# Performance work log

Hardware: AMD Instinct MI355X
Metric: run time of the kernel (lower is better)

## Reference

```python
import jax, jax.numpy as jnp
import numpy as np

OBS, HID, H, A = 128, 256, 512, 16
T, B = 256, 256


def setup_inputs() -> dict:
    key = jax.random.key(0)
    ks = jax.random.split(key, 8)
    s = lambda k, shape, fan_in: jax.random.normal(k, shape, jnp.float32) / np.sqrt(fan_in).astype(np.float32)
    return {
        "x": jax.random.normal(ks[0], (T, B, OBS), jnp.float32),
        "W_enc": s(ks[1], (OBS, HID), OBS),
        "b_enc": jnp.zeros((HID,), jnp.float32),
        "Wi": s(ks[2], (HID, 4 * H), HID),      # input->gates kernel (i,f,g,o)
        "Wh": s(ks[3], (H, 4 * H), H),          # hidden->gates kernel
        "b_lstm": jnp.zeros((4 * H,), jnp.float32),
        "W_mu": s(ks[4], (H, A), H),
        "b_mu": jnp.zeros((A,), jnp.float32),
        "log_std": jnp.zeros((1, A), jnp.float32),
        "W_v": s(ks[5], (H, 1), H),
        "b_v": jnp.zeros((1,), jnp.float32),
    }


def reference(x, W_enc, b_enc, Wi, Wh, b_lstm, W_mu, b_mu, log_std, W_v, b_v):
    # Encoder MLP: Linear + gelu, mapping obs_dim -> hidden_features.
    feats = jax.nn.gelu(x @ W_enc + b_enc)            # (T, B, HID)
    # Precompute the input contribution to all 4 gates for every timestep
    # (same math as flax OptimizedLSTMCell, hoisted out of the scan).
    x_gates = feats @ Wi + b_lstm                      # (T, B, 4H)
    bsz = x.shape[1]
    c0 = jnp.zeros((bsz, H), x.dtype)
    h0 = jnp.zeros((bsz, H), x.dtype)

    def step(carry, xg):
        c, h = carry
        z = xg + h @ Wh                                # (B, 4H)
        i, f, g, o = jnp.split(z, 4, axis=-1)          # flax gate order i,f,g,o
        c_new = jax.nn.sigmoid(f) * c + jax.nn.sigmoid(i) * jnp.tanh(g)
        h_new = jax.nn.sigmoid(o) * jnp.tanh(c_new)
        return (c_new, h_new), h_new

    _, hs = jax.lax.scan(step, (c0, h0), x_gates)      # hs: (T, B, H)
    # Heads (dropout is identity in eval/deterministic mode).
    mu = hs @ W_mu + b_mu                              # (T, B, A)
    sigma = jnp.broadcast_to(jnp.exp(log_std), mu.shape)
    value = hs @ W_v + b_v                             # (T, B, 1)
    return mu, sigma, value
```

## Files before the change

kernel.cpp:

```cpp
#include <hip/hip_runtime.h>
#include <stdint.h>

#define T_STEPS 256
#define BATCH   256
#define OBS     128
#define HID     256
#define HSZ     512
#define NG      16
#define RPG     16
#define NSLICES 16
#define HCS     32
#define RING_SLOT_W 65536

typedef __attribute__((ext_vector_type(8))) short short8;
typedef __attribute__((ext_vector_type(4))) float f32x4;
typedef __attribute__((ext_vector_type(4))) int   i32x4;

__device__ __forceinline__ unsigned short f2bf(float x) {
    union { float f; uint32_t u; } v; v.f = x;
    uint32_t r = v.u + 0x7FFF + ((v.u >> 16) & 1);
    return (unsigned short)(r >> 16);
}
__device__ __forceinline__ float sigmoidf_(float x) { return 1.f / (1.f + __expf(-x)); }
__device__ __forceinline__ float tanhf_(float x)    { return 1.f - 2.f / (1.f + __expf(2.f * x)); }

__global__ __launch_bounds__(256) void enc_kernel(
    const float* __restrict__ x, const float* __restrict__ W_enc,
    const float* __restrict__ b_enc, unsigned short* __restrict__ feats) {
    __shared__ unsigned short wlds[HID * OBS];
    int tid = threadIdx.x;
    for (int idx = tid; idx < OBS * HID; idx += 256) {
        int k = idx >> 8, n = idx & 255;
        int byte = ((n * OBS + k) * 2) ^ ((n & 7) << 4);
        *(unsigned short*)((char*)wlds + byte) = f2bf(W_enc[k * HID + n]);
    }
    __syncthreads();
    int wave = tid >> 6, lane = tid & 63;
    long m0 = (long)blockIdx.x * 64 + wave * 16;
    int arow = lane & 15, kq = lane >> 4;
    f32x4 acc[16];
    f32x4 z4 = {0.f, 0.f, 0.f, 0.f};
#pragma unroll
    for (int i = 0; i < 16; i++) acc[i] = z4;
#pragma unroll
    for (int kk = 0; kk < OBS; kk += 32) {
        const float* ap = x + (m0 + arow) * OBS + kk + kq * 8;
        float4 a0 = *(const float4*)ap;
        float4 a1 = *(const float4*)(ap + 4);
        short8 af;
        af[0] = (short)f2bf(a0.x); af[1] = (short)f2bf(a0.y);
        af[2] = (short)f2bf(a0.z); af[3] = (short)f2bf(a0.w);
        af[4] = (short)f2bf(a1.x); af[5] = (short)f2bf(a1.y);
        af[6] = (short)f2bf(a1.z); af[7] = (short)f2bf(a1.w);
#pragma unroll
        for (int nt = 0; nt < 16; nt++) {
            int n = nt * 16 + arow;
            int byte = ((n * OBS + kk + kq * 8) * 2) ^ ((n & 7) << 4);
            short8 bf = *(const short8*)((char*)wlds + byte);
            acc[nt] = __builtin_amdgcn_mfma_f32_16x16x32_bf16(af, bf, acc[nt], 0, 0, 0);
        }
    }
#pragma unroll
    for (int nt = 0; nt < 16; nt++) {
        int col = nt * 16 + (lane & 15);
        float bias = b_enc[col];
#pragma unroll
        for (int j = 0; j < 4; j++) {
            long row = m0 + kq * 4 + j;
            float z = acc[nt][j] + bias;
            float zc = 0.79788456f * (z + 0.044715f * z * z * z);
            float g = 0.5f * z * (1.f + tanhf_(zc));
            feats[row * HID + col] = f2bf(g);
        }
    }
}

__global__ __launch_bounds__(256) void prep_wi(
    const float* __restrict__ Wi, unsigned short* __restrict__ Wipk) {
    int t = blockIdx.x * 256 + threadIdx.x;
    int f = t & 15, l = (t >> 4) & 63, w = (t >> 10) & 3, s = t >> 12;
    int ct = f >> 3, i = f & 7;
    int n = w * 32 + ct * 16 + (l & 15);
    int colg = (n & 3) * HSZ + s * HCS + (n >> 2);
    int kbase = i * 32 + (l >> 4) * 8;
    short8 v;
#pragma unroll
    for (int j = 0; j < 8; j++) v[j] = (short)f2bf(Wi[(kbase + j) * 2048 + colg]);
    *(short8*)(Wipk + (long)t * 8) = v;
}

__global__ __launch_bounds__(256) void prep_whimg(
    const float* __restrict__ Wh, unsigned short* __restrict__ WhImg) {
    int t = blockIdx.x * 256 + threadIdx.x;
    int s = t >> 15, r = t & 32767;
    int n = r >> 8, k2 = (r & 255) * 2;
    int colg = (n & 3) * HSZ + s * HCS + (n >> 2);
    unsigned short a = f2bf(Wh[k2 * 2048 + colg]);
    unsigned short b = f2bf(Wh[(k2 + 1) * 2048 + colg]);
    uint32_t w = (uint32_t)a | ((uint32_t)b << 16);
    int P = (n * 1024 + k2 * 2) ^ ((n & 7) << 4);
    *(uint32_t*)((char*)WhImg + s * 131072 + P) = w;
}

__global__ __launch_bounds__(256, 1) void scan_kernel(
    const float* __restrict__ b_lstm, const unsigned short* __restrict__ feats,
    const unsigned short* __restrict__ Wipk, const unsigned short* __restrict__ WhImg,
    uint32_t* __restrict__ ring, uint32_t* __restrict__ flags,
    uint32_t* __restrict__ hs32) {
    __shared__ unsigned short whs[128 * HSZ];
    __shared__ unsigned short hst[RPG * HSZ];
    const int tid = threadIdx.x;
    const int g = blockIdx.x & 15;
    const int slice = blockIdx.x >> 4;
    const int rowg = g * RPG;
    const int wave = tid >> 6, lane = tid & 63;
    const int arow = lane & 15, kq = lane >> 4;

    {
        const i32x4* src = (const i32x4*)((const char*)WhImg + slice * 131072);
        i32x4* dst = (i32x4*)whs;
        for (int idx = tid; idx < 8192; idx += 256) dst[idx] = src[idx];
    }
    short8 wif0[8], wif1[8];
    {
        const short8* wp = (const short8*)Wipk + ((slice * 4 + wave) * 64 + lane) * 16;
#pragma unroll
        for (int i = 0; i < 8; i++) { wif0[i] = wp[i]; wif1[i] = wp[8 + i]; }
    }
    const int a_ = arow >> 2;
    const int hcol0 = slice * HCS + wave * 8 + a_;
    float bl0[4], bl1[4];
#pragma unroll
    for (int q = 0; q < 4; q++) {
        bl0[q] = b_lstm[q * HSZ + hcol0];
        bl1[q] = b_lstm[q * HSZ + hcol0 + 4];
    }
    const int row = kq * 4 + (arow & 3);
    const int colw = slice * 16 + wave * 4 + ((a_ & 1) ? 2 + (a_ >> 1) : (a_ >> 1));
    float c0 = 0.f, c1 = 0.f;
    int wb[4];
#pragma unroll
    for (int j = 0; j < 4; j++) {
        int rj = j * 4 + wave;
        wb[j] = (rj * 1024 + lane * 16) ^ ((rj & 7) << 4);
    }
    short8 ff[8];
    {
        const char* fb = (const char*)feats + ((long)(rowg + arow)) * (HID * 2) + kq * 16;
#pragma unroll
        for (int i = 0; i < 8; i++) ff[i] = *(const short8*)(fb + i * 64);
    }
    f32x4 z4 = {0.f, 0.f, 0.f, 0.f};
    __syncthreads();

    for (int t = 0; t < T_STEPS; ++t) {
        f32x4 acc0 = z4, acc1 = z4;
#pragma unroll
        for (int i = 0; i < 8; i++) {
            acc0 = __builtin_amdgcn_mfma_f32_16x16x32_bf16(ff[i], wif0[i], acc0, 0, 0, 0);
            acc1 = __builtin_amdgcn_mfma_f32_16x16x32_bf16(ff[i], wif1[i], acc1, 0, 0, 0);
        }
        {
            int tn = (t + 1 < T_STEPS) ? t + 1 : t;
            const char* fb = (const char*)feats
                           + ((long)tn * BATCH + rowg + arow) * (HID * 2) + kq * 16;
#pragma unroll
            for (int i = 0; i < 8; i++) ff[i] = *(const short8*)(fb + i * 64);
        }
        __builtin_amdgcn_sched_barrier(0);
        if (t > 0) {
            const uint32_t* fp = flags + ((long)g * T_STEPS + t - 1) * 16 + (lane & 15);
            while (!__all(__hip_atomic_load(fp, __ATOMIC_RELAXED,
                                            __HIP_MEMORY_SCOPE_AGENT) != 0u)) {}
            __builtin_amdgcn_sched_barrier(0);
            const char* rb = (const char*)ring + ((t - 1) & 3) * (RING_SLOT_W * 4)
                           + (rowg + wave) * 1024 + lane * 16;
            i32x4 S0, S1, S2, S3;
            asm volatile(
                "global_load_dwordx4 %0, %4, off sc0 sc1\n\t"
                "global_load_dwordx4 %1, %5, off sc0 sc1\n\t"
                "global_load_dwordx4 %2, %6, off sc0 sc1\n\t"
                "global_load_dwordx4 %3, %7, off sc0 sc1"
                : "=&v"(S0), "=&v"(S1), "=&v"(S2), "=&v"(S3)
                : "v"(rb), "v"(rb + 4096), "v"(rb + 8192), "v"(rb + 12288));
            asm volatile("s_waitcnt vmcnt(0)" ::: "memory");
            __builtin_amdgcn_sched_barrier(0);
            *(i32x4*)((char*)hst + wb[0]) = S0;
            *(i32x4*)((char*)hst + wb[1]) = S1;
            *(i32x4*)((char*)hst + wb[2]) = S2;
            *(i32x4*)((char*)hst + wb[3]) = S3;
            __syncthreads();
            const int n0 = wave * 32 + arow, n1 = n0 + 16;
#pragma unroll
            for (int i = 0; i < 16; i++) {
                short8 ah = *(const short8*)((char*)hst
                              + ((arow * 1024 + i * 64 + kq * 16) ^ ((arow & 7) << 4)));
                short8 b0 = *(const short8*)((char*)whs
                              + ((n0 * 1024 + i * 64 + kq * 16) ^ ((n0 & 7) << 4)));
                short8 b1 = *(const short8*)((char*)whs
                              + ((n1 * 1024 + i * 64 + kq * 16) ^ ((n1 & 7) << 4)));
                acc0 = __builtin_amdgcn_mfma_f32_16x16x32_bf16(ah, b0, acc0, 0, 0, 0);
                acc1 = __builtin_amdgcn_mfma_f32_16x16x32_bf16(ah, b1, acc1, 0, 0, 0);
            }
        }
        float C0, C1, C2, C3, D0, D1, D2, D3;
        {
            float s0 = __shfl_xor(acc0[0], 1), s1 = __shfl_xor(acc0[1], 1);
            float s2 = __shfl_xor(acc0[2], 1), s3 = __shfl_xor(acc0[3], 1);
            bool o1 = arow & 1;
            float b0_ = o1 ? s1 : acc0[0], b1_ = o1 ? acc0[1] : s0;
            float b2_ = o1 ? s3 : acc0[2], b3_ = o1 ? acc0[3] : s2;
            float r0 = __shfl_xor(b0_, 2), r1 = __shfl_xor(b1_, 2);
            float r2 = __shfl_xor(b2_, 2), r3 = __shfl_xor(b3_, 2);
            bool o2 = arow & 2;
            C0 = o2 ? r2 : b0_; C1 = o2 ? r3 : b1_;
            C2 = o2 ? b2_ : r0; C3 = o2 ? b3_ : r1;
            s0 = __shfl_xor(acc1[0], 1); s1 = __shfl_xor(acc1[1], 1);
            s2 = __shfl_xor(acc1[2], 1); s3 = __shfl_xor(acc1[3], 1);
            b0_ = o1 ? s1 : acc1[0]; b1_ = o1 ? acc1[1] : s0;
            b2_ = o1 ? s3 : acc1[2]; b3_ = o1 ? acc1[3] : s2;
            r0 = __shfl_xor(b0_, 2); r1 = __shfl_xor(b1_, 2);
            r2 = __shfl_xor(b2_, 2); r3 = __shfl_xor(b3_, 2);
            D0 = o2 ? r2 : b0_; D1 = o2 ? r3 : b1_;
            D2 = o2 ? b2_ : r0; D3 = o2 ? b3_ : r1;
        }
        c0 = sigmoidf_(C1 + bl0[1]) * c0 + sigmoidf_(C0 + bl0[0]) * tanhf_(C2 + bl0[2]);
        c1 = sigmoidf_(D1 + bl1[1]) * c1 + sigmoidf_(D0 + bl1[0]) * tanhf_(D2 + bl1[2]);
        float h0 = sigmoidf_(C3 + bl0[3]) * tanhf_(c0);
        float h1 = sigmoidf_(D3 + bl1[3]) * tanhf_(c1);
        uint32_t hu0 = f2bf(h0), hu1 = f2bf(h1);
        uint32_t p0 = (uint32_t)__shfl_xor((int)hu0, 4);
        uint32_t p1 = (uint32_t)__shfl_xor((int)hu1, 4);
        uint32_t word = (a_ & 1) ? (p1 | (hu1 << 16)) : (hu0 | (p0 << 16));
        uint32_t* wp = ring + (t & 3) * RING_SLOT_W + (rowg + row) * 256 + colw;
        asm volatile("global_store_dword %0, %1, off sc0 sc1" :: "v"(wp), "v"(word) : "memory");
        hs32[((long)t * BATCH + rowg + row) * 256 + colw] = word;
        __syncthreads();
        if (tid == 0) {
            uint32_t one = 1;
            const uint32_t* fq = flags + ((long)g * T_STEPS + t) * 16 + slice;
            asm volatile("global_store_dword %0, %1, off sc0 sc1" :: "v"(fq), "v"(one) : "memory");
        }
    }
}

__global__ __launch_bounds__(256) void heads_kernel(
    const unsigned short* __restrict__ hs, const float* __restrict__ W_mu,
    const float* __restrict__ b_mu, const float* __restrict__ log_std,
    const float* __restrict__ W_v, const float* __restrict__ b_v,
    float* __restrict__ mu_out, float* __restrict__ sig_out,
    float* __restrict__ val_out) {
    __shared__ unsigned short wlds[32 * HSZ];
    int tid = threadIdx.x;
    for (int idx = tid; idx < 32 * HSZ; idx += 256) {
        int n = idx & 31, k = idx >> 5;
        float w = 0.f;
        if (n < 16) w = W_mu[k * 16 + n];
        else if (n == 16) w = W_v[k];
        int byte = ((n * HSZ + k) * 2) ^ ((n & 7) << 4);
        *(unsigned short*)((char*)wlds + byte) = f2bf(w);
    }
    __syncthreads();
    int wave = tid >> 6, lane = tid & 63;
    long m0 = (long)blockIdx.x * 64 + wave * 16;
    int arow = lane & 15, kq = lane >> 4;
    f32x4 acc0 = {0.f, 0.f, 0.f, 0.f}, acc1 = {0.f, 0.f, 0.f, 0.f};
    const unsigned short* hr = hs + (m0 + arow) * HSZ + kq * 8;
#pragma unroll
    for (int kk = 0; kk < HSZ; kk += 32) {
        short8 af = *(const short8*)(hr + kk);
        int n0 = arow;
        int b0 = ((n0 * HSZ + kk + kq * 8) * 2) ^ ((n0 & 7) << 4);
        short8 bf0 = *(const short8*)((char*)wlds + b0);
        acc0 = __builtin_amdgcn_mfma_f32_16x16x32_bf16(af, bf0, acc0, 0, 0, 0);
        int n1 = 16 + arow;
        int b1 = ((n1 * HSZ + kk + kq * 8) * 2) ^ ((n1 & 7) << 4);
        short8 bf1 = *(const short8*)((char*)wlds + b1);
        acc1 = __builtin_amdgcn_mfma_f32_16x16x32_bf16(af, bf1, acc1, 0, 0, 0);
    }
    int col = lane & 15;
    float bm = b_mu[col];
    float sg = __expf(log_std[col]);
#pragma unroll
    for (int j = 0; j < 4; j++) {
        long row = m0 + kq * 4 + j;
        mu_out[row * 16 + col]  = acc0[j] + bm;
        sig_out[row * 16 + col] = sg;
    }
    if (col == 0) {
        float bv = b_v[0];
#pragma unroll
        for (int j = 0; j < 4; j++) {
            long row = m0 + kq * 4 + j;
            val_out[row] = acc1[j] + bv;
        }
    }
}

extern "C" void kernel_launch(void* const* d_in, const int* in_sizes, int n_in,
                              void* d_out, int out_size, void* d_ws, size_t ws_size,
                              hipStream_t stream) {
    const float* x      = (const float*)d_in[0];
    const float* W_enc  = (const float*)d_in[1];
    const float* b_enc  = (const float*)d_in[2];
    const float* Wi     = (const float*)d_in[3];
    const float* Wh     = (const float*)d_in[4];
    const float* b_lstm = (const float*)d_in[5];
    const float* W_mu   = (const float*)d_in[6];
    const float* b_mu   = (const float*)d_in[7];
    const float* lstd   = (const float*)d_in[8];
    const float* W_v    = (const float*)d_in[9];
    const float* b_v    = (const float*)d_in[10];

    char* ws = (char*)d_ws;
    uint32_t*       ring  = (uint32_t*)ws;
    uint32_t*       flags = (uint32_t*)(ws + (1 << 20));
    unsigned short* Wipk  = (unsigned short*)(ws + (2 << 20));
    unsigned short* WhImg = (unsigned short*)(ws + (3 << 20));
    unsigned short* feats = (unsigned short*)(ws + (5 << 20));
    unsigned short* hs    = (unsigned short*)(ws + (5 << 20) + 33554432);

    float* mu_out  = (float*)d_out;
    float* sig_out = mu_out + 1048576;
    float* val_out = mu_out + 2097152;

    hipMemsetAsync(flags, 0, (size_t)NG * T_STEPS * 16 * sizeof(uint32_t), stream);
    prep_wi<<<dim3(256), dim3(256), 0, stream>>>(Wi, Wipk);
    prep_whimg<<<dim3(2048), dim3(256), 0, stream>>>(Wh, WhImg);
    enc_kernel<<<dim3(1024), dim3(256), 0, stream>>>(x, W_enc, b_enc, feats);
    scan_kernel<<<dim3(256), dim3(256), 0, stream>>>(b_lstm, feats, Wipk, WhImg,
                                                     ring, flags, (uint32_t*)hs);
    heads_kernel<<<dim3(1024), dim3(256), 0, stream>>>(hs, W_mu, b_mu, lstd, W_v, b_v,
                                                       mu_out, sig_out, val_out);
}
```

Measured before the change: 889.4 us.

## Split LSTM scan across 32 column slices with 512 persistent blocks

Halves the hidden columns handled per scan block (16 instead of 32), doubling the grid to 512 blocks and allowing two blocks per CU. Each block now holds half the Wh slice in LDS and does half the MFMA work per step, shortening the per-step critical path. The flag wait now polls 32 flags with an explicit uncached load. In exchange there is more inter-block synchronisation traffic per step, and the two co-resident persistent blocks per CU are relied on to all be resident for the spin-wait scheme to avoid deadlock.

```diff
diff --git a/kernel.cpp b/kernel.cpp
--- a/kernel.cpp
+++ b/kernel.cpp
@@ -8,8 +8,9 @@
 #define HSZ     512
 #define NG      16
 #define RPG     16
-#define NSLICES 16
-#define HCS     32
+#define NSLICES 32
+#define HCS     16
+#define GCOLS   64
 #define RING_SLOT_W 65536
 
 typedef __attribute__((ext_vector_type(8))) short short8;
@@ -78,9 +79,8 @@
 __global__ __launch_bounds__(256) void prep_wi(
     const float* __restrict__ Wi, unsigned short* __restrict__ Wipk) {
     int t = blockIdx.x * 256 + threadIdx.x;
-    int f = t & 15, l = (t >> 4) & 63, w = (t >> 10) & 3, s = t >> 12;
-    int ct = f >> 3, i = f & 7;
-    int n = w * 32 + ct * 16 + (l & 15);
+    int i = t & 7, l = (t >> 3) & 63, w = (t >> 9) & 3, s = t >> 11;
+    int n = w * 16 + (l & 15);
     int colg = (n & 3) * HSZ + s * HCS + (n >> 2);
     int kbase = i * 32 + (l >> 4) * 8;
     short8 v;
@@ -92,22 +92,22 @@
 __global__ __launch_bounds__(256) void prep_whimg(
     const float* __restrict__ Wh, unsigned short* __restrict__ WhImg) {
     int t = blockIdx.x * 256 + threadIdx.x;
-    int s = t >> 15, r = t & 32767;
+    int s = t >> 14, r = t & 16383;
     int n = r >> 8, k2 = (r & 255) * 2;
     int colg = (n & 3) * HSZ + s * HCS + (n >> 2);
     unsigned short a = f2bf(Wh[k2 * 2048 + colg]);
     unsigned short b = f2bf(Wh[(k2 + 1) * 2048 + colg]);
     uint32_t w = (uint32_t)a | ((uint32_t)b << 16);
     int P = (n * 1024 + k2 * 2) ^ ((n & 7) << 4);
-    *(uint32_t*)((char*)WhImg + s * 131072 + P) = w;
-}
-
-__global__ __launch_bounds__(256, 1) void scan_kernel(
+    *(uint32_t*)((char*)WhImg + s * 65536 + P) = w;
+}
+
+__global__ __launch_bounds__(256, 2) void scan_kernel(
     const float* __restrict__ b_lstm, const unsigned short* __restrict__ feats,
     const unsigned short* __restrict__ Wipk, const unsigned short* __restrict__ WhImg,
     uint32_t* __restrict__ ring, uint32_t* __restrict__ flags,
     uint32_t* __restrict__ hs32) {
-    __shared__ unsigned short whs[128 * HSZ];
+    __shared__ unsigned short whs[GCOLS * HSZ];
     __shared__ unsigned short hst[RPG * HSZ];
     const int tid = threadIdx.x;
     const int g = blockIdx.x & 15;
@@ -117,27 +117,24 @@
     const int arow = lane & 15, kq = lane >> 4;
 
     {
-        const i32x4* src = (const i32x4*)((const char*)WhImg + slice * 131072);
+        const i32x4* src = (const i32x4*)((const char*)WhImg + slice * 65536);
         i32x4* dst = (i32x4*)whs;
-        for (int idx = tid; idx < 8192; idx += 256) dst[idx] = src[idx];
-    }
-    short8 wif0[8], wif1[8];
+        for (int idx = tid; idx < 4096; idx += 256) dst[idx] = src[idx];
+    }
+    short8 wif0[8];
     {
-        const short8* wp = (const short8*)Wipk + ((slice * 4 + wave) * 64 + lane) * 16;
-#pragma unroll
-        for (int i = 0; i < 8; i++) { wif0[i] = wp[i]; wif1[i] = wp[8 + i]; }
+        const short8* wp = (const short8*)Wipk + ((slice * 4 + wave) * 64 + lane) * 8;
+#pragma unroll
+        for (int i = 0; i < 8; i++) wif0[i] = wp[i];
     }
     const int a_ = arow >> 2;
-    const int hcol0 = slice * HCS + wave * 8 + a_;
-    float bl0[4], bl1[4];
-#pragma unroll
-    for (int q = 0; q < 4; q++) {
-        bl0[q] = b_lstm[q * HSZ + hcol0];
-        bl1[q] = b_lstm[q * HSZ + hcol0 + 4];
-    }
+    const int hcol0 = slice * HCS + wave * 4 + a_;
+    float bl0[4];
+#pragma unroll
+    for (int q = 0; q < 4; q++) bl0[q] = b_lstm[q * HSZ + hcol0];
     const int row = kq * 4 + (arow & 3);
-    const int colw = slice * 16 + wave * 4 + ((a_ & 1) ? 2 + (a_ >> 1) : (a_ >> 1));
-    float c0 = 0.f, c1 = 0.f;
+    const int colw = slice * 8 + wave * 2 + (a_ >> 1);
+    float c0 = 0.f;
     int wb[4];
 #pragma unroll
     for (int j = 0; j < 4; j++) {
@@ -154,12 +151,10 @@
     __syncthreads();
 
     for (int t = 0; t < T_STEPS; ++t) {
-        f32x4 acc0 = z4, acc1 = z4;
-#pragma unroll
-        for (int i = 0; i < 8; i++) {
+        f32x4 acc0 = z4;
+#pragma unroll
+        for (int i = 0; i < 8; i++)
             acc0 = __builtin_amdgcn_mfma_f32_16x16x32_bf16(ff[i], wif0[i], acc0, 0, 0, 0);
-            acc1 = __builtin_amdgcn_mfma_f32_16x16x32_bf16(ff[i], wif1[i], acc1, 0, 0, 0);
-        }
         {
             int tn = (t + 1 < T_STEPS) ? t + 1 : t;
             const char* fb = (const char*)feats
@@ -169,9 +164,14 @@
         }
         __builtin_amdgcn_sched_barrier(0);
         if (t > 0) {
-            const uint32_t* fp = flags + ((long)g * T_STEPS + t - 1) * 16 + (lane & 15);
-            while (!__all(__hip_atomic_load(fp, __ATOMIC_RELAXED,
-                                            __HIP_MEMORY_SCOPE_AGENT) != 0u)) {}
+            const uint32_t* fp = flags + ((long)g * T_STEPS + t - 1) * 32 + (lane & 31);
+            uint32_t got;
+            do {
+                got = 1u;
+                if (lane < 32)
+                    asm volatile("global_load_dword %0, %1, off sc0 sc1\n\t"
+                                 "s_waitcnt vmcnt(0)" : "=&v"(got) : "v"(fp));
+            } while (!__all(got != 0));
             __builtin_amdgcn_sched_barrier(0);
             const char* rb = (const char*)ring + ((t - 1) & 3) * (RING_SLOT_W * 4)
                            + (rowg + wave) * 1024 + lane * 16;
@@ -190,20 +190,17 @@
             *(i32x4*)((char*)hst + wb[2]) = S2;
             *(i32x4*)((char*)hst + wb[3]) = S3;
             __syncthreads();
-            const int n0 = wave * 32 + arow, n1 = n0 + 16;
+            const int n0 = wave * 16 + arow;
 #pragma unroll
             for (int i = 0; i < 16; i++) {
                 short8 ah = *(const short8*)((char*)hst
                               + ((arow * 1024 + i * 64 + kq * 16) ^ ((arow & 7) << 4)));
                 short8 b0 = *(const short8*)((char*)whs
                               + ((n0 * 1024 + i * 64 + kq * 16) ^ ((n0 & 7) << 4)));
-                short8 b1 = *(const short8*)((char*)whs
-                              + ((n1 * 1024 + i * 64 + kq * 16) ^ ((n1 & 7) << 4)));
                 acc0 = __builtin_amdgcn_mfma_f32_16x16x32_bf16(ah, b0, acc0, 0, 0, 0);
-                acc1 = __builtin_amdgcn_mfma_f32_16x16x32_bf16(ah, b1, acc1, 0, 0, 0);
             }
         }
-        float C0, C1, C2, C3, D0, D1, D2, D3;
+        float C0, C1, C2, C3;
         {
             float s0 = __shfl_xor(acc0[0], 1), s1 = __shfl_xor(acc0[1], 1);
             float s2 = __shfl_xor(acc0[2], 1), s3 = __shfl_xor(acc0[3], 1);
@@ -215,30 +212,21 @@
             bool o2 = arow & 2;
             C0 = o2 ? r2 : b0_; C1 = o2 ? r3 : b1_;
             C2 = o2 ? b2_ : r0; C3 = o2 ? b3_ : r1;
-            s0 = __shfl_xor(acc1[0], 1); s1 = __shfl_xor(acc1[1], 1);
-            s2 = __shfl_xor(acc1[2], 1); s3 = __shfl_xor(acc1[3], 1);
-            b0_ = o1 ? s1 : acc1[0]; b1_ = o1 ? acc1[1] : s0;
-            b2_ = o1 ? s3 : acc1[2]; b3_ = o1 ? acc1[3] : s2;
-            r0 = __shfl_xor(b0_, 2); r1 = __shfl_xor(b1_, 2);
-            r2 = __shfl_xor(b2_, 2); r3 = __shfl_xor(b3_, 2);
-            D0 = o2 ? r2 : b0_; D1 = o2 ? r3 : b1_;
-            D2 = o2 ? b2_ : r0; D3 = o2 ? b3_ : r1;
         }
         c0 = sigmoidf_(C1 + bl0[1]) * c0 + sigmoidf_(C0 + bl0[0]) * tanhf_(C2 + bl0[2]);
-        c1 = sigmoidf_(D1 + bl1[1]) * c1 + sigmoidf_(D0 + bl1[0]) * tanhf_(D2 + bl1[2]);
         float h0 = sigmoidf_(C3 + bl0[3]) * tanhf_(c0);
-        float h1 = sigmoidf_(D3 + bl1[3]) * tanhf_(c1);
-        uint32_t hu0 = f2bf(h0), hu1 = f2bf(h1);
+        uint32_t hu0 = f2bf(h0);
         uint32_t p0 = (uint32_t)__shfl_xor((int)hu0, 4);
-        uint32_t p1 = (uint32_t)__shfl_xor((int)hu1, 4);
-        uint32_t word = (a_ & 1) ? (p1 | (hu1 << 16)) : (hu0 | (p0 << 16));
-        uint32_t* wp = ring + (t & 3) * RING_SLOT_W + (rowg + row) * 256 + colw;
-        asm volatile("global_store_dword %0, %1, off sc0 sc1" :: "v"(wp), "v"(word) : "memory");
-        hs32[((long)t * BATCH + rowg + row) * 256 + colw] = word;
+        if ((a_ & 1) == 0) {
+            uint32_t word = hu0 | (p0 << 16);
+            uint32_t* wp = ring + (t & 3) * RING_SLOT_W + (rowg + row) * 256 + colw;
+            asm volatile("global_store_dword %0, %1, off sc0 sc1" :: "v"(wp), "v"(word) : "memory");
+            hs32[((long)t * BATCH + rowg + row) * 256 + colw] = word;
+        }
         __syncthreads();
         if (tid == 0) {
             uint32_t one = 1;
-            const uint32_t* fq = flags + ((long)g * T_STEPS + t) * 16 + slice;
+            const uint32_t* fq = flags + ((long)g * T_STEPS + t) * 32 + slice;
             asm volatile("global_store_dword %0, %1, off sc0 sc1" :: "v"(fq), "v"(one) : "memory");
         }
     }
@@ -324,11 +312,11 @@
     float* sig_out = mu_out + 1048576;
     float* val_out = mu_out + 2097152;
 
-    hipMemsetAsync(flags, 0, (size_t)NG * T_STEPS * 16 * sizeof(uint32_t), stream);
+    hipMemsetAsync(flags, 0, (size_t)NG * T_STEPS * 32 * sizeof(uint32_t), stream);
     prep_wi<<<dim3(256), dim3(256), 0, stream>>>(Wi, Wipk);
     prep_whimg<<<dim3(2048), dim3(256), 0, stream>>>(Wh, WhImg);
     enc_kernel<<<dim3(1024), dim3(256), 0, stream>>>(x, W_enc, b_enc, feats);
-    scan_kernel<<<dim3(256), dim3(256), 0, stream>>>(b_lstm, feats, Wipk, WhImg,
+    scan_kernel<<<dim3(512), dim3(256), 0, stream>>>(b_lstm, feats, Wipk, WhImg,
                                                      ring, flags, (uint32_t*)hs);
     heads_kernel<<<dim3(1024), dim3(256), 0, stream>>>(hs, W_mu, b_mu, lstd, W_v, b_v,
                                                        mu_out, sig_out, val_out);
```

Measured after the change: 1.511 ms. +69.9%, slower.

## Replace block barriers with per-wave byte flags and direct register h loads

Applied to the files above, without the earlier changes.

Each wave now publishes its own byte flag after its ring store completes. Consumers poll a packed dword of four wave flags per slice, so the block-wide __syncthreads before signalling is gone. The h-state A operand is loaded straight from the ring into registers in MFMA layout, which removes the LDS staging buffer and its barrier. The next-step feature prefetch is moved after the store so it overlaps the inter-block wait. In exchange, each wave issues more global loads of h per step, 16 instead of 4, which adds redundant ring traffic.

```diff
diff --git a/kernel.cpp b/kernel.cpp
--- a/kernel.cpp
+++ b/kernel.cpp
@@ -10,6 +10,7 @@
 #define RPG     16
 #define NSLICES 16
 #define HCS     32
+#define GCOLS   128
 #define RING_SLOT_W 65536
 
 typedef __attribute__((ext_vector_type(8))) short short8;
@@ -23,6 +24,13 @@
 }
 __device__ __forceinline__ float sigmoidf_(float x) { return 1.f / (1.f + __expf(-x)); }
 __device__ __forceinline__ float tanhf_(float x)    { return 1.f - 2.f / (1.f + __expf(2.f * x)); }
+
+#define GLD4(d0, d1, d2, d3, p, O0, O1, O2, O3)                                 \
+    asm volatile("global_load_dwordx4 %0, %4, off offset:" #O0 " sc0 sc1\n\t"   \
+                 "global_load_dwordx4 %1, %4, off offset:" #O1 " sc0 sc1\n\t"   \
+                 "global_load_dwordx4 %2, %4, off offset:" #O2 " sc0 sc1\n\t"   \
+                 "global_load_dwordx4 %3, %4, off offset:" #O3 " sc0 sc1"       \
+                 : "=&v"(d0), "=&v"(d1), "=&v"(d2), "=&v"(d3) : "v"(p))
 
 __global__ __launch_bounds__(256) void enc_kernel(
     const float* __restrict__ x, const float* __restrict__ W_enc,
@@ -105,10 +113,9 @@
 __global__ __launch_bounds__(256, 1) void scan_kernel(
     const float* __restrict__ b_lstm, const unsigned short* __restrict__ feats,
     const unsigned short* __restrict__ Wipk, const unsigned short* __restrict__ WhImg,
-    uint32_t* __restrict__ ring, uint32_t* __restrict__ flags,
+    uint32_t* __restrict__ ring, unsigned char* __restrict__ flagsB,
     uint32_t* __restrict__ hs32) {
     __shared__ unsigned short whs[128 * HSZ];
-    __shared__ unsigned short hst[RPG * HSZ];
     const int tid = threadIdx.x;
     const int g = blockIdx.x & 15;
     const int slice = blockIdx.x >> 4;
@@ -138,12 +145,6 @@
     const int row = kq * 4 + (arow & 3);
     const int colw = slice * 16 + wave * 4 + ((a_ & 1) ? 2 + (a_ >> 1) : (a_ >> 1));
     float c0 = 0.f, c1 = 0.f;
-    int wb[4];
-#pragma unroll
-    for (int j = 0; j < 4; j++) {
-        int rj = j * 4 + wave;
-        wb[j] = (rj * 1024 + lane * 16) ^ ((rj & 7) << 4);
-    }
     short8 ff[8];
     {
         const char* fb = (const char*)feats + ((long)(rowg + arow)) * (HID * 2) + kq * 16;
@@ -160,45 +161,33 @@
             acc0 = __builtin_amdgcn_mfma_f32_16x16x32_bf16(ff[i], wif0[i], acc0, 0, 0, 0);
             acc1 = __builtin_amdgcn_mfma_f32_16x16x32_bf16(ff[i], wif1[i], acc1, 0, 0, 0);
         }
-        {
-            int tn = (t + 1 < T_STEPS) ? t + 1 : t;
-            const char* fb = (const char*)feats
-                           + ((long)tn * BATCH + rowg + arow) * (HID * 2) + kq * 16;
-#pragma unroll
-            for (int i = 0; i < 8; i++) ff[i] = *(const short8*)(fb + i * 64);
-        }
         __builtin_amdgcn_sched_barrier(0);
         if (t > 0) {
-            const uint32_t* fp = flags + ((long)g * T_STEPS + t - 1) * 16 + (lane & 15);
-            while (!__all(__hip_atomic_load(fp, __ATOMIC_RELAXED,
-                                            __HIP_MEMORY_SCOPE_AGENT) != 0u)) {}
+            const uint32_t* fl = (const uint32_t*)(flagsB + ((long)g * T_STEPS + t - 1) * 64)
+                               + (lane & 15);
+            uint32_t fv;
+            do {
+                asm volatile("global_load_dword %0, %1, off sc0 sc1\n\t"
+                             "s_waitcnt vmcnt(0)" : "=&v"(fv) : "v"(fl));
+            } while (!__all(fv == 0x01010101u));
             __builtin_amdgcn_sched_barrier(0);
             const char* rb = (const char*)ring + ((t - 1) & 3) * (RING_SLOT_W * 4)
-                           + (rowg + wave) * 1024 + lane * 16;
-            i32x4 S0, S1, S2, S3;
-            asm volatile(
-                "global_load_dwordx4 %0, %4, off sc0 sc1\n\t"
-                "global_load_dwordx4 %1, %5, off sc0 sc1\n\t"
-                "global_load_dwordx4 %2, %6, off sc0 sc1\n\t"
-                "global_load_dwordx4 %3, %7, off sc0 sc1"
-                : "=&v"(S0), "=&v"(S1), "=&v"(S2), "=&v"(S3)
-                : "v"(rb), "v"(rb + 4096), "v"(rb + 8192), "v"(rb + 12288));
+                           + (rowg + arow) * 1024 + kq * 16;
+            i32x4 H[16];
+            GLD4(H[0],  H[1],  H[2],  H[3],  rb, 0,   64,  128, 192);
+            GLD4(H[4],  H[5],  H[6],  H[7],  rb, 256, 320, 384, 448);
+            GLD4(H[8],  H[9],  H[10], H[11], rb, 512, 576, 640, 704);
+            GLD4(H[12], H[13], H[14], H[15], rb, 768, 832, 896, 960);
             asm volatile("s_waitcnt vmcnt(0)" ::: "memory");
             __builtin_amdgcn_sched_barrier(0);
-            *(i32x4*)((char*)hst + wb[0]) = S0;
-            *(i32x4*)((char*)hst + wb[1]) = S1;
-            *(i32x4*)((char*)hst + wb[2]) = S2;
-            *(i32x4*)((char*)hst + wb[3]) = S3;
-            __syncthreads();
             const int n0 = wave * 32 + arow, n1 = n0 + 16;
 #pragma unroll
             for (int i = 0; i < 16; i++) {
-                short8 ah = *(const short8*)((char*)hst
-                              + ((arow * 1024 + i * 64 + kq * 16) ^ ((arow & 7) << 4)));
                 short8 b0 = *(const short8*)((char*)whs
                               + ((n0 * 1024 + i * 64 + kq * 16) ^ ((n0 & 7) << 4)));
                 short8 b1 = *(const short8*)((char*)whs
                               + ((n1 * 1024 + i * 64 + kq * 16) ^ ((n1 & 7) << 4)));
+                short8 ah = __builtin_bit_cast(short8, H[i]);
                 acc0 = __builtin_amdgcn_mfma_f32_16x16x32_bf16(ah, b0, acc0, 0, 0, 0);
                 acc1 = __builtin_amdgcn_mfma_f32_16x16x32_bf16(ah, b1, acc1, 0, 0, 0);
             }
@@ -234,12 +223,19 @@
         uint32_t word = (a_ & 1) ? (p1 | (hu1 << 16)) : (hu0 | (p0 << 16));
         uint32_t* wp = ring + (t & 3) * RING_SLOT_W + (rowg + row) * 256 + colw;
         asm volatile("global_store_dword %0, %1, off sc0 sc1" :: "v"(wp), "v"(word) : "memory");
+        asm volatile("s_waitcnt vmcnt(0)" ::: "memory");
+        if (lane == 0) {
+            unsigned char* fb = flagsB + ((long)g * T_STEPS + t) * 64 + slice * 4 + wave;
+            uint32_t one = 1;
+            asm volatile("global_store_byte %0, %1, off sc0 sc1" :: "v"(fb), "v"(one) : "memory");
+        }
         hs32[((long)t * BATCH + rowg + row) * 256 + colw] = word;
-        __syncthreads();
-        if (tid == 0) {
-            uint32_t one = 1;
-            const uint32_t* fq = flags + ((long)g * T_STEPS + t) * 16 + slice;
-            asm volatile("global_store_dword %0, %1, off sc0 sc1" :: "v"(fq), "v"(one) : "memory");
+        {
+            int tn = (t + 1 < T_STEPS) ? t + 1 : t;
+            const char* fb2 = (const char*)feats
+                            + ((long)tn * BATCH + rowg + arow) * (HID * 2) + kq * 16;
+#pragma unroll
+            for (int i = 0; i < 8; i++) ff[i] = *(const short8*)(fb2 + i * 64);
         }
     }
 }
@@ -313,23 +309,23 @@
     const float* b_v    = (const float*)d_in[10];
 
     char* ws = (char*)d_ws;
-    uint32_t*       ring  = (uint32_t*)ws;
-    uint32_t*       flags = (uint32_t*)(ws + (1 << 20));
-    unsigned short* Wipk  = (unsigned short*)(ws + (2 << 20));
-    unsigned short* WhImg = (unsigned short*)(ws + (3 << 20));
-    unsigned short* feats = (unsigned short*)(ws + (5 << 20));
-    unsigned short* hs    = (unsigned short*)(ws + (5 << 20) + 33554432);
+    uint32_t*       ring   = (uint32_t*)ws;
+    unsigned char*  flagsB = (unsigned char*)(ws + (1 << 20));
+    unsigned short* Wipk   = (unsigned short*)(ws + (2 << 20));
+    unsigned short* WhImg  = (unsigned short*)(ws + (3 << 20));
+    unsigned short* feats  = (unsigned short*)(ws + (5 << 20));
+    unsigned short* hs     = (unsigned short*)(ws + (5 << 20) + 33554432);
 
     float* mu_out  = (float*)d_out;
     float* sig_out = mu_out + 1048576;
     float* val_out = mu_out + 2097152;
 
-    hipMemsetAsync(flags, 0, (size_t)NG * T_STEPS * 16 * sizeof(uint32_t), stream);
+    hipMemsetAsync(flagsB, 0, (size_t)NG * T_STEPS * 64, stream);
     prep_wi<<<dim3(256), dim3(256), 0, stream>>>(Wi, Wipk);
     prep_whimg<<<dim3(2048), dim3(256), 0, stream>>>(Wh, WhImg);
     enc_kernel<<<dim3(1024), dim3(256), 0, stream>>>(x, W_enc, b_enc, feats);
     scan_kernel<<<dim3(256), dim3(256), 0, stream>>>(b_lstm, feats, Wipk, WhImg,
-                                                     ring, flags, (uint32_t*)hs);
+                                                     ring, flagsB, (uint32_t*)hs);
     heads_kernel<<<dim3(1024), dim3(256), 0, stream>>>(hs, W_mu, b_mu, lstd, W_v, b_v,
                                                        mu_out, sig_out, val_out);
 }
```

After: 1.682 ms. 89.1% more time.
